# Optimization experiments

Hardware: AMD Instinct MI355X
Metric: run time of the kernel (lower is better)

Reference implementation:

```python
import jax, jax.numpy as jnp
import numpy as np
import math

D_MODEL = 1024
N_HEAD = 16
D_HEAD = D_MODEL // N_HEAD  # 64
D_KMAP = 128
B, L = 4, 4096


def setup_inputs() -> dict:
    key = jax.random.key(0)
    ks = jax.random.split(key, 10)
    s = 1.0 / math.sqrt(D_MODEL)
    inp = {
        "x": jax.random.normal(ks[0], (B, L, D_MODEL), dtype=jnp.float32),
        "proj_mat": jax.random.normal(ks[1], (D_HEAD, D_KMAP), dtype=jnp.float32),
        "Wq": jax.random.uniform(ks[2], (D_MODEL, D_MODEL), minval=-s, maxval=s),
        "bq": jax.random.uniform(ks[3], (D_MODEL,), minval=-s, maxval=s),
        "Wk": jax.random.uniform(ks[4], (D_MODEL, D_MODEL), minval=-s, maxval=s),
        "bk": jax.random.uniform(ks[5], (D_MODEL,), minval=-s, maxval=s),
        "Wv": jax.random.uniform(ks[6], (D_MODEL, D_MODEL), minval=-s, maxval=s),
        "bv": jax.random.uniform(ks[7], (D_MODEL,), minval=-s, maxval=s),
        "Wo": jax.random.uniform(ks[8], (D_MODEL, D_MODEL), minval=-s, maxval=s),
        "bo": jax.random.uniform(ks[9], (D_MODEL,), minval=-s, maxval=s),
    }
    return inp


def _fourier_kernel(x, proj_mat):
    # x: [B,L,H,d_head] -> [B,L,H,2*d_kmap]
    p = jnp.einsum("blhd,dm->blhm", x, proj_mat) / math.sqrt(D_HEAD)
    return jnp.concatenate([jnp.cos(p), jnp.sin(p)], axis=-1) / math.sqrt(D_KMAP)


def reference(x, proj_mat, Wq, bq, Wk, bk, Wv, bv, Wo, bo):
    Bv, Lv, _ = x.shape
    q = (x @ Wq.T + bq).reshape(Bv, Lv, N_HEAD, D_HEAD)
    k = (x @ Wk.T + bk).reshape(Bv, Lv, N_HEAD, D_HEAD)
    v = (x @ Wv.T + bv).reshape(Bv, Lv, N_HEAD, D_HEAD)
    q_prime = _fourier_kernel(q, proj_mat)  # [B,L,H,2M]
    k_prime = _fourier_kernel(k, proj_mat)  # [B,L,H,2M]
    kv = jnp.einsum("blhm,blhd->bhmd", k_prime, v)  # [B,H,2M,d_head]
    out = jnp.einsum("blhm,bhmd->blhd", q_prime, kv)  # [B,L,H,d_head]
    out = out.reshape(Bv, Lv, D_MODEL)
    return out @ Wo.T + bo
```

## Files before the change

kernel.cpp:

```cpp
#include <hip/hip_runtime.h>
#include <cstddef>
#include <cstdint>


typedef __attribute__((ext_vector_type(8))) short s8v;
typedef __attribute__((ext_vector_type(4))) short s4v;
typedef __attribute__((ext_vector_type(4))) float f32x4;

#define MFMA_BF16(a, b, c) __builtin_amdgcn_mfma_f32_16x16x32_bf16((a), (b), (c), 0, 0, 0)

#define P_SCALE 0.125f
#define F_SCALE 0.08838834764831845f

static __device__ __forceinline__ unsigned short f2bf(float f) {
  unsigned int u = __float_as_uint(f);
  u += 0x7fffu + ((u >> 16) & 1u);
  return (unsigned short)(u >> 16);
}

static __device__ __forceinline__ void gload_lds16(const void* g, void* l) {
  __builtin_amdgcn_global_load_lds(
      (const __attribute__((address_space(1))) unsigned int*)g,
      (__attribute__((address_space(3))) unsigned int*)l, 16, 0, 0);
}

__global__ void conv_all_kernel(const float* __restrict__ x,
                                const float* __restrict__ Wq, const float* __restrict__ Wk,
                                const float* __restrict__ Wv, const float* __restrict__ Wo,
                                const float* __restrict__ proj,
                                short* __restrict__ xb, short* __restrict__ Wqkvb,
                                short* __restrict__ Wob, short* __restrict__ projT) {
  const int T = blockIdx.x * 256 + threadIdx.x;
  for (int u = T; u < 5244928; u += 524288) {
    if (u < 4194304) {
      float4 f = ((const float4*)x)[u];
      s4v v;
      v[0] = (short)f2bf(f.x); v[1] = (short)f2bf(f.y);
      v[2] = (short)f2bf(f.z); v[3] = (short)f2bf(f.w);
      ((s4v*)xb)[u] = v;
    } else if (u < 5242880) {
      int vi = u - 4194304;
      int wi = vi >> 18;
      int off = vi & 262143;
      const float* src = (wi == 0) ? Wq : (wi == 1) ? Wk : (wi == 2) ? Wv : Wo;
      short* dst = (wi < 3) ? (Wqkvb + (size_t)wi * 1048576) : Wob;
      float4 f = ((const float4*)src)[off];
      s4v v;
      v[0] = (short)f2bf(f.x); v[1] = (short)f2bf(f.y);
      v[2] = (short)f2bf(f.z); v[3] = (short)f2bf(f.w);
      ((s4v*)dst)[off] = v;
    } else {
      int vi = u - 5242880;
      int d = vi >> 5, m4 = (vi & 31) * 4;
      float4 f = ((const float4*)proj)[vi];
      projT[(m4 + 0) * 64 + d] = (short)f2bf(f.x);
      projT[(m4 + 1) * 64 + d] = (short)f2bf(f.y);
      projT[(m4 + 2) * 64 + d] = (short)f2bf(f.z);
      projT[(m4 + 3) * 64 + d] = (short)f2bf(f.w);
    }
  }
}

__global__ void qkv_gemm_kernel(const short* __restrict__ xb,
                                const short* __restrict__ Wqkv,
                                const float* __restrict__ bq_, const float* __restrict__ bk_,
                                const float* __restrict__ bv_,
                                short* __restrict__ qb, short* __restrict__ kb,
                                short* __restrict__ vT, int bn_base) {
  __shared__ __align__(16) short smem[17408];
  short* Al = smem;
  short* Bl = smem + 8192;

  const int t = threadIdx.x;
  const int bm = blockIdx.x, bn = blockIdx.y + bn_base;
  const int row0 = bm * 128, n0 = bn * 128;
  const int lane = t & 63, w = t >> 6;
  const int wm = w & 1, wn = w >> 1;
  const int l15 = lane & 15, lq = lane >> 4;
  const int sx = (l15 & 7) * 8;

  f32x4 acc[4][4];
#pragma unroll
  for (int i = 0; i < 4; ++i)
#pragma unroll
    for (int j = 0; j < 4; ++j) acc[i][j] = (f32x4){0.f, 0.f, 0.f, 0.f};

  for (int k0 = 0; k0 < 1024; k0 += 64) {
#pragma unroll
    for (int i = 0; i < 4; ++i) {
      int c = t + i * 256;
      int r = c >> 3, cl = c & 7;
      int cg = cl ^ (r & 7);
      gload_lds16(xb   + (size_t)(row0 + r) * 1024 + k0 + cg * 8, Al + c * 8);
      gload_lds16(Wqkv + (size_t)(n0 + r) * 1024 + k0 + cg * 8, Bl + c * 8);
    }
    __syncthreads();
#pragma unroll
    for (int ks = 0; ks < 2; ++ks) {
      const int kb8 = (ks * 4 + lq) * 8;
      s8v af[4], bfr[4];
#pragma unroll
      for (int i = 0; i < 4; ++i)
        af[i] = *(s8v*)&Al[(wm * 64 + i * 16 + l15) * 64 + (kb8 ^ sx)];
#pragma unroll
      for (int j = 0; j < 4; ++j)
        bfr[j] = *(s8v*)&Bl[(wn * 64 + j * 16 + l15) * 64 + (kb8 ^ sx)];
#pragma unroll
      for (int i = 0; i < 4; ++i)
#pragma unroll
        for (int j = 0; j < 4; ++j)
          acc[i][j] = MFMA_BF16(af[i], bfr[j], acc[i][j]);
    }
    __syncthreads();
  }

  const int region = bn >> 3;
  if (region < 2) {
    const float* bias = (region == 0) ? bq_ : bk_;
    short* IM = smem;
#pragma unroll
    for (int j = 0; j < 4; ++j) {
      int cl = wn * 64 + j * 16 + l15;
      float bsv = bias[(n0 & 1023) + cl];
#pragma unroll
      for (int i = 0; i < 4; ++i)
#pragma unroll
        for (int r = 0; r < 4; ++r)
          IM[(wm * 64 + i * 16 + lq * 4 + r) * 136 + cl] = (short)f2bf(acc[i][j][r] + bsv);
    }
    __syncthreads();
    short* dst = (region == 0) ? qb : kb;
#pragma unroll
    for (int i = 0; i < 8; ++i) {
      int c = t + i * 256;
      int r = c >> 4, cc = c & 15;
      *(s8v*)&dst[(size_t)(row0 + r) * 1024 + (n0 & 1023) + cc * 8] =
          *(s8v*)&IM[r * 136 + cc * 8];
    }
  } else {
    short* IM = smem;
#pragma unroll
    for (int j = 0; j < 4; ++j) {
      int cl = wn * 64 + j * 16 + l15;
      float bsv = bv_[(n0 - 2048) + cl];
#pragma unroll
      for (int i = 0; i < 4; ++i) {
        s4v pk;
#pragma unroll
        for (int r = 0; r < 4; ++r) pk[r] = (short)f2bf(acc[i][j][r] + bsv);
        *(s4v*)&IM[cl * 136 + wm * 64 + i * 16 + lq * 4] = pk;
      }
    }
    __syncthreads();
    const int b = row0 >> 12;
    const int l0 = (bm & 31) * 128;
#pragma unroll
    for (int i = 0; i < 8; ++i) {
      int c = t + i * 256;
      int ci = c >> 4, cc = c & 15;
      int cv = (bn - 16) * 128 + ci;
      int grow = (b * 16 + (cv >> 6)) * 64 + (cv & 63);
      *(s8v*)&vT[(size_t)grow * 4096 + l0 + cc * 8] = *(s8v*)&IM[ci * 136 + cc * 8];
    }
  }
}

__global__ void kv_accum_kernel(const short* __restrict__ kb, const short* __restrict__ vT,
                                const short* __restrict__ projT, float* __restrict__ kv) {
  __shared__ __align__(16) short smem[26624];
  short* kt = smem;
  short* vt = smem + 4096;
  short* kpT = smem + 8192;

  const int t = threadIdx.x;
  const int bid = blockIdx.x;
  const int chunk = bid & 7, h = (bid >> 3) & 15, b = bid >> 7;
  const int lane = t & 63, w = t >> 6;
  const int l15 = lane & 15, lq = lane >> 4;
  const int sx = (l15 & 7) * 8;

  s8v pf[8][2];
#pragma unroll
  for (int nt = 0; nt < 8; ++nt)
#pragma unroll
    for (int ks = 0; ks < 2; ++ks)
      pf[nt][ks] = *(const s8v*)(projT + (size_t)(nt * 16 + l15) * 64 + ks * 32 + lq * 8);

  f32x4 kvacc[4][4];
#pragma unroll
  for (int i = 0; i < 4; ++i)
#pragma unroll
    for (int j = 0; j < 4; ++j) kvacc[i][j] = (f32x4){0.f, 0.f, 0.f, 0.f};

  for (int s = 0; s < 8; ++s) {
    const int l0s = chunk * 512 + s * 64;
#pragma unroll
    for (int i = 0; i < 2; ++i) {
      int c = t + i * 256;
      int r = c >> 3, cl = c & 7;
      int cg = cl ^ (r & 7);
      gload_lds16(kb + (size_t)(b * 4096 + l0s + r) * 1024 + h * 64 + cg * 8, kt + c * 8);
      gload_lds16(vT + (size_t)((b * 16 + h) * 64 + r) * 4096 + l0s + cg * 8, vt + c * 8);
    }
    __syncthreads();

    f32x4 pacc[8];
#pragma unroll
    for (int nt = 0; nt < 8; ++nt) pacc[nt] = (f32x4){0.f, 0.f, 0.f, 0.f};
#pragma unroll
    for (int ks = 0; ks < 2; ++ks) {
      const int kb8 = (ks * 4 + lq) * 8;
      s8v af = *(s8v*)&kt[(w * 16 + l15) * 64 + (kb8 ^ sx)];
#pragma unroll
      for (int nt = 0; nt < 8; ++nt) pacc[nt] = MFMA_BF16(af, pf[nt][ks], pacc[nt]);
    }
#pragma unroll
    for (int nt = 0; nt < 8; ++nt) {
      s4v cp, sp;
#pragma unroll
      for (int r = 0; r < 4; ++r) {
        float pv = pacc[nt][r] * P_SCALE;
        float sv, cv;
        __sincosf(pv, &sv, &cv);
        cp[r] = (short)f2bf(cv * F_SCALE);
        sp[r] = (short)f2bf(sv * F_SCALE);
      }
      int m = nt * 16 + l15;
      int rbase = w * 16 + lq * 4;
      *(s4v*)&kpT[m * 72 + rbase] = cp;
      *(s4v*)&kpT[(m + 128) * 72 + rbase] = sp;
    }
    __syncthreads();

#pragma unroll
    for (int ks = 0; ks < 2; ++ks) {
      const int kb8 = (ks * 4 + lq) * 8;
      s8v af[4], bf4[4];
#pragma unroll
      for (int i = 0; i < 4; ++i)
        af[i] = *(s8v*)&kpT[(w * 64 + i * 16 + l15) * 72 + ks * 32 + lq * 8];
#pragma unroll
      for (int j = 0; j < 4; ++j)
        bf4[j] = *(s8v*)&vt[(j * 16 + l15) * 64 + (kb8 ^ sx)];
#pragma unroll
      for (int i = 0; i < 4; ++i)
#pragma unroll
        for (int j = 0; j < 4; ++j)
          kvacc[i][j] = MFMA_BF16(af[i], bf4[j], kvacc[i][j]);
    }
    __syncthreads();
  }

  float* kvb = kv + (size_t)chunk * 1048576 + ((size_t)(b * 16 + h) << 14);
#pragma unroll
  for (int i = 0; i < 4; ++i)
#pragma unroll
    for (int j = 0; j < 4; ++j)
#pragma unroll
      for (int r = 0; r < 4; ++r) {
        int m = w * 64 + i * 16 + lq * 4 + r;
        int d = j * 16 + l15;
        kvb[(size_t)m * 64 + d] = kvacc[i][j][r];
      }
}

__global__ void kvT_kernel(const float* __restrict__ kvp, short* __restrict__ kvT) {
  __shared__ __align__(16) short im[4608];
  const int t = threadIdx.x;
  const int bh = blockIdx.x, mc = blockIdx.y;
  const float* base = kvp + (size_t)bh * 16384 + (size_t)mc * 4096;
#pragma unroll
  for (int i = 0; i < 4; ++i) {
    int idx4 = t + i * 256;
    int mm = idx4 >> 4, d4 = (idx4 & 15) * 4;
    float4 s = {0.f, 0.f, 0.f, 0.f};
#pragma unroll
    for (int c = 0; c < 8; ++c) {
      float4 v = *(const float4*)(base + (size_t)c * 1048576 + mm * 64 + d4);
      s.x += v.x; s.y += v.y; s.z += v.z; s.w += v.w;
    }
    im[(d4 + 0) * 72 + mm] = (short)f2bf(s.x);
    im[(d4 + 1) * 72 + mm] = (short)f2bf(s.y);
    im[(d4 + 2) * 72 + mm] = (short)f2bf(s.z);
    im[(d4 + 3) * 72 + mm] = (short)f2bf(s.w);
  }
  __syncthreads();
#pragma unroll
  for (int i = 0; i < 2; ++i) {
    int c = t + i * 256;
    int d = c >> 3, mm8 = (c & 7) * 8;
    *(s8v*)&kvT[(size_t)(bh * 64 + d) * 256 + mc * 64 + mm8] = *(s8v*)&im[d * 72 + mm8];
  }
}

__global__ void attn_kernel(const short* __restrict__ qb, const short* __restrict__ projT,
                            const short* __restrict__ kvT, short* __restrict__ attnb) {
  __shared__ __align__(16) short smem[20992];
  short* qt = smem;
  short* qA = smem + 4096;
  short* kvt = smem + 12800;

  const int t = threadIdx.x;
  const int rt = blockIdx.x, h = blockIdx.y;
  const int row0 = rt * 64;
  const int b = row0 >> 12;
  const int lane = t & 63, w = t >> 6;
  const int l15 = lane & 15, lq = lane >> 4;
  const int sx = (l15 & 7) * 8;

  s8v pf[8][2];
#pragma unroll
  for (int nt = 0; nt < 8; ++nt)
#pragma unroll
    for (int ks = 0; ks < 2; ++ks)
      pf[nt][ks] = *(const s8v*)(projT + (size_t)(nt * 16 + l15) * 64 + ks * 32 + lq * 8);

#pragma unroll
  for (int i = 0; i < 2; ++i) {
    int c = t + i * 256;
    int r = c >> 3, cl = c & 7;
    int cg = cl ^ (r & 7);
    gload_lds16(qb + (size_t)(row0 + r) * 1024 + h * 64 + cg * 8, qt + c * 8);
  }
  __syncthreads();

  f32x4 pacc[8];
#pragma unroll
  for (int nt = 0; nt < 8; ++nt) pacc[nt] = (f32x4){0.f, 0.f, 0.f, 0.f};
#pragma unroll
  for (int ks = 0; ks < 2; ++ks) {
    const int kb8 = (ks * 4 + lq) * 8;
    s8v af = *(s8v*)&qt[(w * 16 + l15) * 64 + (kb8 ^ sx)];
#pragma unroll
    for (int nt = 0; nt < 8; ++nt) pacc[nt] = MFMA_BF16(af, pf[nt][ks], pacc[nt]);
  }

  f32x4 aacc[4];
#pragma unroll
  for (int j = 0; j < 4; ++j) aacc[j] = (f32x4){0.f, 0.f, 0.f, 0.f};

#pragma unroll
  for (int half = 0; half < 2; ++half) {
#pragma unroll
    for (int nt = 0; nt < 8; ++nt)
#pragma unroll
      for (int r = 0; r < 4; ++r) {
        float p = pacc[nt][r] * P_SCALE;
        float fv = (half == 0) ? __cosf(p) : __sinf(p);
        qA[(w * 16 + lq * 4 + r) * 136 + nt * 16 + l15] = (short)f2bf(fv * F_SCALE);
      }
#pragma unroll
    for (int i = 0; i < 4; ++i) {
      int c = t + i * 256;
      int d = c >> 4, cl = c & 15;
      int cg = cl ^ (d & 15);
      gload_lds16(kvT + (size_t)((b * 16 + h) * 64 + d) * 256 + half * 128 + cg * 8,
                  kvt + c * 8);
    }
    __syncthreads();
#pragma unroll
    for (int ks = 0; ks < 4; ++ks) {
      s8v af = *(s8v*)&qA[(w * 16 + l15) * 136 + ks * 32 + lq * 8];
#pragma unroll
      for (int j = 0; j < 4; ++j) {
        int row = j * 16 + l15;
        s8v bf4 = *(s8v*)&kvt[row * 128 + (((ks * 4 + lq) ^ l15) * 8)];
        aacc[j] = MFMA_BF16(af, bf4, aacc[j]);
      }
    }
    __syncthreads();
  }

#pragma unroll
  for (int j = 0; j < 4; ++j)
#pragma unroll
    for (int r = 0; r < 4; ++r)
      smem[(w * 16 + lq * 4 + r) * 72 + j * 16 + l15] = (short)f2bf(aacc[j][r]);
  __syncthreads();
#pragma unroll
  for (int i = 0; i < 2; ++i) {
    int c = t + i * 256;
    int r = c >> 3, cc = c & 7;
    *(s8v*)&attnb[(size_t)(row0 + r) * 1024 + h * 64 + cc * 8] = *(s8v*)&smem[r * 72 + cc * 8];
  }
}

__global__ void out_gemm_kernel(const short* __restrict__ attnb, const short* __restrict__ Wob,
                                const float* __restrict__ bo_, float* __restrict__ out) {
  __shared__ __align__(16) short smem[16384];
  short* Al = smem;
  short* Bl = smem + 8192;

  const int t = threadIdx.x;
  const int bm = blockIdx.x, bn = blockIdx.y;
  const int row0 = bm * 128, n0 = bn * 128;
  const int lane = t & 63, w = t >> 6;
  const int wm = w & 1, wn = w >> 1;
  const int l15 = lane & 15, lq = lane >> 4;
  const int sx = (l15 & 7) * 8;

  f32x4 acc[4][4];
#pragma unroll
  for (int i = 0; i < 4; ++i)
#pragma unroll
    for (int j = 0; j < 4; ++j) acc[i][j] = (f32x4){0.f, 0.f, 0.f, 0.f};

  for (int k0 = 0; k0 < 1024; k0 += 64) {
#pragma unroll
    for (int i = 0; i < 4; ++i) {
      int c = t + i * 256;
      int r = c >> 3, cl = c & 7;
      int cg = cl ^ (r & 7);
      gload_lds16(attnb + (size_t)(row0 + r) * 1024 + k0 + cg * 8, Al + c * 8);
      gload_lds16(Wob   + (size_t)(n0 + r) * 1024 + k0 + cg * 8, Bl + c * 8);
    }
    __syncthreads();
#pragma unroll
    for (int ks = 0; ks < 2; ++ks) {
      const int kb8 = (ks * 4 + lq) * 8;
      s8v af[4], bfr[4];
#pragma unroll
      for (int i = 0; i < 4; ++i)
        af[i] = *(s8v*)&Al[(wm * 64 + i * 16 + l15) * 64 + (kb8 ^ sx)];
#pragma unroll
      for (int j = 0; j < 4; ++j)
        bfr[j] = *(s8v*)&Bl[(wn * 64 + j * 16 + l15) * 64 + (kb8 ^ sx)];
#pragma unroll
      for (int i = 0; i < 4; ++i)
#pragma unroll
        for (int j = 0; j < 4; ++j)
          acc[i][j] = MFMA_BF16(af[i], bfr[j], acc[i][j]);
    }
    __syncthreads();
  }

#pragma unroll
  for (int j = 0; j < 4; ++j) {
    int cl = wn * 64 + j * 16 + l15;
    float bsv = bo_[n0 + cl];
#pragma unroll
    for (int i = 0; i < 4; ++i)
#pragma unroll
      for (int r = 0; r < 4; ++r)
        out[(size_t)(row0 + wm * 64 + i * 16 + lq * 4 + r) * 1024 + n0 + cl] =
            acc[i][j][r] + bsv;
  }
}

extern "C" void kernel_launch(void* const* d_in, const int* in_sizes, int n_in,
                              void* d_out, int out_size, void* d_ws, size_t ws_size,
                              hipStream_t stream) {
  const float* x    = (const float*)d_in[0];
  const float* proj = (const float*)d_in[1];
  const float* Wq   = (const float*)d_in[2];
  const float* bq   = (const float*)d_in[3];
  const float* Wk   = (const float*)d_in[4];
  const float* bk   = (const float*)d_in[5];
  const float* Wv   = (const float*)d_in[6];
  const float* bv   = (const float*)d_in[7];
  const float* Wo   = (const float*)d_in[8];
  const float* bo   = (const float*)d_in[9];
  float* out = (float*)d_out;

  char* wsb = (char*)d_ws;
  short* qb    = (short*)(wsb + 0);
  short* kb    = (short*)(wsb + 33554432);
  short* vT    = (short*)(wsb + 67108864);
  short* xb    = (short*)(wsb + 100663296);
  short* Wqkvb = (short*)(wsb + 134217728);
  short* Wob   = (short*)(wsb + 140509184);
  short* projT = (short*)(wsb + 142606336);
  float* kv_part = (float*)(wsb + 100663296);
  short* attnb = kb;
  short* kvT   = vT;

  conv_all_kernel<<<dim3(2048), dim3(256), 0, stream>>>(
      x, Wq, Wk, Wv, Wo, proj, xb, Wqkvb, Wob, projT);

  qkv_gemm_kernel<<<dim3(128, 12), dim3(256), 0, stream>>>(
      xb, Wqkvb, bq, bk, bv, qb, kb, vT, 0);
  qkv_gemm_kernel<<<dim3(128, 12), dim3(256), 0, stream>>>(
      xb, Wqkvb, bq, bk, bv, qb, kb, vT, 12);
  kv_accum_kernel<<<dim3(512), dim3(256), 0, stream>>>(kb, vT, projT, kv_part);
  kvT_kernel<<<dim3(64, 4), dim3(256), 0, stream>>>(kv_part, kvT);
  attn_kernel<<<dim3(256, 16), dim3(256), 0, stream>>>(qb, projT, kvT, attnb);
  out_gemm_kernel<<<dim3(128, 8), dim3(256), 0, stream>>>(attnb, Wob, bo, out);
}
```

Measured before the change: 403.7 us.

## Store Q/K/attn head-major and V in 64-row supertiles for contiguous tile loads

Intermediate Q, K and attention buffers change from row-major [B*L,1024] to head-major [B,H,L,64]. V is written as [B,H,L/64,64,64] supertiles. Every 64x64 tile the downstream kernels load is then one contiguous 8KB block instead of 64 strided 128-byte pieces. This targets DRAM/TLB locality in the kv_accum, attn and out_gemm loads, at the cost of more scattered stores in the QKV GEMM epilogue.

```diff
diff --git a/kernel.cpp b/kernel.cpp
--- a/kernel.cpp
+++ b/kernel.cpp
@@ -65,8 +65,8 @@
                                 const short* __restrict__ Wqkv,
                                 const float* __restrict__ bq_, const float* __restrict__ bk_,
                                 const float* __restrict__ bv_,
-                                short* __restrict__ qb, short* __restrict__ kb,
-                                short* __restrict__ vT, int bn_base) {
+                                short* __restrict__ qh, short* __restrict__ kh,
+                                short* __restrict__ vS, int bn_base) {
   __shared__ __align__(16) short smem[17408];
   short* Al = smem;
   short* Bl = smem + 8192;
@@ -114,6 +114,8 @@
     __syncthreads();
   }
 
+  const int b = row0 >> 12;
+  const int Lloc = row0 & 4095;
   const int region = bn >> 3;
   if (region < 2) {
     const float* bias = (region == 0) ? bq_ : bk_;
@@ -129,12 +131,15 @@
           IM[(wm * 64 + i * 16 + lq * 4 + r) * 136 + cl] = (short)f2bf(acc[i][j][r] + bsv);
     }
     __syncthreads();
-    short* dst = (region == 0) ? qb : kb;
+    short* dst = (region == 0) ? qh : kh;
+    const int h0 = (n0 & 1023) >> 6;
 #pragma unroll
     for (int i = 0; i < 8; ++i) {
       int c = t + i * 256;
       int r = c >> 4, cc = c & 15;
-      *(s8v*)&dst[(size_t)(row0 + r) * 1024 + (n0 & 1023) + cc * 8] =
+      int h = h0 + (cc >> 3);
+      int d0 = (cc & 7) * 8;
+      *(s8v*)&dst[((size_t)(b * 16 + h) * 4096 + Lloc + r) * 64 + d0] =
           *(s8v*)&IM[r * 136 + cc * 8];
     }
   } else {
@@ -152,20 +157,22 @@
       }
     }
     __syncthreads();
-    const int b = row0 >> 12;
-    const int l0 = (bm & 31) * 128;
+    const int sup0 = Lloc >> 6;
 #pragma unroll
     for (int i = 0; i < 8; ++i) {
       int c = t + i * 256;
       int ci = c >> 4, cc = c & 15;
       int cv = (bn - 16) * 128 + ci;
-      int grow = (b * 16 + (cv >> 6)) * 64 + (cv & 63);
-      *(s8v*)&vT[(size_t)grow * 4096 + l0 + cc * 8] = *(s8v*)&IM[ci * 136 + cc * 8];
-    }
-  }
-}
-
-__global__ void kv_accum_kernel(const short* __restrict__ kb, const short* __restrict__ vT,
+      int h = cv >> 6, d = cv & 63;
+      int sup = sup0 + (cc >> 3);
+      int Loff = (cc & 7) * 8;
+      *(s8v*)&vS[((((size_t)(b * 16 + h) * 64 + sup) * 64 + d) * 64) + Loff] =
+          *(s8v*)&IM[ci * 136 + cc * 8];
+    }
+  }
+}
+
+__global__ void kv_accum_kernel(const short* __restrict__ kh, const short* __restrict__ vS,
                                 const short* __restrict__ projT, float* __restrict__ kv) {
   __shared__ __align__(16) short smem[26624];
   short* kt = smem;
@@ -179,6 +186,9 @@
   const int l15 = lane & 15, lq = lane >> 4;
   const int sx = (l15 & 7) * 8;
 
+  const short* khb = kh + (size_t)(b * 16 + h) * 4096 * 64;
+  const short* vsb = vS + (size_t)(b * 16 + h) * 64 * 4096;
+
   s8v pf[8][2];
 #pragma unroll
   for (int nt = 0; nt < 8; ++nt)
@@ -194,13 +204,14 @@
 
   for (int s = 0; s < 8; ++s) {
     const int l0s = chunk * 512 + s * 64;
+    const int sup = l0s >> 6;
 #pragma unroll
     for (int i = 0; i < 2; ++i) {
       int c = t + i * 256;
       int r = c >> 3, cl = c & 7;
       int cg = cl ^ (r & 7);
-      gload_lds16(kb + (size_t)(b * 4096 + l0s + r) * 1024 + h * 64 + cg * 8, kt + c * 8);
-      gload_lds16(vT + (size_t)((b * 16 + h) * 64 + r) * 4096 + l0s + cg * 8, vt + c * 8);
+      gload_lds16(khb + (size_t)(l0s + r) * 64 + cg * 8, kt + c * 8);
+      gload_lds16(vsb + (size_t)sup * 4096 + r * 64 + cg * 8, vt + c * 8);
     }
     __syncthreads();
 
@@ -293,7 +304,7 @@
   }
 }
 
-__global__ void attn_kernel(const short* __restrict__ qb, const short* __restrict__ projT,
+__global__ void attn_kernel(const short* __restrict__ qh, const short* __restrict__ projT,
                             const short* __restrict__ kvT, short* __restrict__ attnb) {
   __shared__ __align__(16) short smem[20992];
   short* qt = smem;
@@ -304,9 +315,12 @@
   const int rt = blockIdx.x, h = blockIdx.y;
   const int row0 = rt * 64;
   const int b = row0 >> 12;
+  const int Lloc = row0 & 4095;
   const int lane = t & 63, w = t >> 6;
   const int l15 = lane & 15, lq = lane >> 4;
   const int sx = (l15 & 7) * 8;
+
+  const short* qhb = qh + (size_t)(b * 16 + h) * 4096 * 64;
 
   s8v pf[8][2];
 #pragma unroll
@@ -320,7 +334,7 @@
     int c = t + i * 256;
     int r = c >> 3, cl = c & 7;
     int cg = cl ^ (r & 7);
-    gload_lds16(qb + (size_t)(row0 + r) * 1024 + h * 64 + cg * 8, qt + c * 8);
+    gload_lds16(qhb + (size_t)(Lloc + r) * 64 + cg * 8, qt + c * 8);
   }
   __syncthreads();
 
@@ -381,7 +395,8 @@
   for (int i = 0; i < 2; ++i) {
     int c = t + i * 256;
     int r = c >> 3, cc = c & 7;
-    *(s8v*)&attnb[(size_t)(row0 + r) * 1024 + h * 64 + cc * 8] = *(s8v*)&smem[r * 72 + cc * 8];
+    *(s8v*)&attnb[((size_t)(b * 16 + h) * 4096 + Lloc + r) * 64 + cc * 8] =
+        *(s8v*)&smem[r * 72 + cc * 8];
   }
 }
 
@@ -394,6 +409,7 @@
   const int t = threadIdx.x;
   const int bm = blockIdx.x, bn = blockIdx.y;
   const int row0 = bm * 128, n0 = bn * 128;
+  const int b4 = row0 >> 12, Ll = row0 & 4095;
   const int lane = t & 63, w = t >> 6;
   const int wm = w & 1, wn = w >> 1;
   const int l15 = lane & 15, lq = lane >> 4;
@@ -406,13 +422,14 @@
     for (int j = 0; j < 4; ++j) acc[i][j] = (f32x4){0.f, 0.f, 0.f, 0.f};
 
   for (int k0 = 0; k0 < 1024; k0 += 64) {
+    const short* Ab = attnb + ((size_t)(b4 * 16 + (k0 >> 6)) * 4096 + Ll) * 64;
 #pragma unroll
     for (int i = 0; i < 4; ++i) {
       int c = t + i * 256;
       int r = c >> 3, cl = c & 7;
       int cg = cl ^ (r & 7);
-      gload_lds16(attnb + (size_t)(row0 + r) * 1024 + k0 + cg * 8, Al + c * 8);
-      gload_lds16(Wob   + (size_t)(n0 + r) * 1024 + k0 + cg * 8, Bl + c * 8);
+      gload_lds16(Ab + (size_t)r * 64 + cg * 8, Al + c * 8);
+      gload_lds16(Wob + (size_t)(n0 + r) * 1024 + k0 + cg * 8, Bl + c * 8);
     }
     __syncthreads();
 #pragma unroll
@@ -463,26 +480,26 @@
   float* out = (float*)d_out;
 
   char* wsb = (char*)d_ws;
-  short* qb    = (short*)(wsb + 0);
-  short* kb    = (short*)(wsb + 33554432);
-  short* vT    = (short*)(wsb + 67108864);
+  short* qh    = (short*)(wsb + 0);
+  short* kh    = (short*)(wsb + 33554432);
+  short* vS    = (short*)(wsb + 67108864);
   short* xb    = (short*)(wsb + 100663296);
   short* Wqkvb = (short*)(wsb + 134217728);
   short* Wob   = (short*)(wsb + 140509184);
   short* projT = (short*)(wsb + 142606336);
   float* kv_part = (float*)(wsb + 100663296);
-  short* attnb = kb;
-  short* kvT   = vT;
+  short* attnb = kh;
+  short* kvT   = vS;
 
   conv_all_kernel<<<dim3(2048), dim3(256), 0, stream>>>(
       x, Wq, Wk, Wv, Wo, proj, xb, Wqkvb, Wob, projT);
 
   qkv_gemm_kernel<<<dim3(128, 12), dim3(256), 0, stream>>>(
-      xb, Wqkvb, bq, bk, bv, qb, kb, vT, 0);
+      xb, Wqkvb, bq, bk, bv, qh, kh, vS, 0);
   qkv_gemm_kernel<<<dim3(128, 12), dim3(256), 0, stream>>>(
-      xb, Wqkvb, bq, bk, bv, qb, kb, vT, 12);
-  kv_accum_kernel<<<dim3(512), dim3(256), 0, stream>>>(kb, vT, projT, kv_part);
+      xb, Wqkvb, bq, bk, bv, qh, kh, vS, 12);
+  kv_accum_kernel<<<dim3(512), dim3(256), 0, stream>>>(kh, vS, projT, kv_part);
   kvT_kernel<<<dim3(64, 4), dim3(256), 0, stream>>>(kv_part, kvT);
-  attn_kernel<<<dim3(256, 16), dim3(256), 0, stream>>>(qb, projT, kvT, attnb);
+  attn_kernel<<<dim3(256, 16), dim3(256), 0, stream>>>(qh, projT, kvT, attnb);
   out_gemm_kernel<<<dim3(128, 8), dim3(256), 0, stream>>>(attnb, Wob, bo, out);
 }
```

Result: slower. 422.6 us (+4.7%).
